# Kernel optimization log

Measured on AMD Instinct MI355X. Metric: run time of the kernel, lower is better.

## Reference

```python
import jax, jax.numpy as jnp
import numpy as np

B, T, C, H, K = 16, 8192, 128, 128, 5


def setup_inputs() -> dict:
    key = jax.random.key(0)
    ks = jax.random.split(key, 6)
    std = 1.0 / np.sqrt(H)  # matches reset_parameters uniform(-std, std)
    u = lambda k, s: jax.random.uniform(k, s, jnp.float32, -std, std)
    return {
        "inputs": jax.random.normal(ks[0], (B, T, C), jnp.float32),
        "init_state": jax.random.normal(ks[1], (2, B, H), jnp.float32),
        "z_w": u(ks[2], (H, C, K)),
        "z_b": u(ks[3], (H,)),
        "f_w": u(ks[4], (H, C, K)),
        "f_b": u(ks[5], (H,)),
    }


def _conv1d_same(x, w, b):
    # x: (B, C, T), w: (H, C, K) -> (B, H, T), padding='same'
    y = jax.lax.conv_general_dilated(
        x, w, window_strides=(1,), padding="SAME",
        dimension_numbers=("NCH", "OIH", "NCH"))
    return y + b[None, :, None]


def reference(inputs, init_state, z_w, z_b, f_w, f_b):
    # inputs: (B, T, C); init_state: (2, B, H)
    x = jnp.transpose(inputs, (0, 2, 1))                       # (B, C, T)
    raw_f = jnp.transpose(_conv1d_same(x, f_w, f_b), (0, 2, 1))  # (B, T, H)
    raw_z = jnp.transpose(_conv1d_same(x, z_w, z_b), (0, 2, 1))  # (B, T, H)
    # prepend init state along time -> (B, T+1, H)
    raw_f = jnp.concatenate([init_state[0][:, None, :], raw_f], axis=1)
    raw_z = jnp.concatenate([init_state[1][:, None, :], raw_z], axis=1)
    log_one_minus_f = jax.nn.log_sigmoid(-raw_f)  # mode='f'
    log_z = jax.nn.log_sigmoid(raw_z)
    log_f = jax.nn.log_sigmoid(raw_f)
    cs = jnp.cumsum(log_f, axis=1)
    # recurrent_gates[t] = log_f[t] - cumsum[t] + cumsum[-1]
    rg = log_f - cs + cs[:, -1:, :]
    log_hidden = jax.lax.cumlogsumexp(log_z + log_one_minus_f + rg, axis=1)
    return jnp.exp(log_hidden - rg)  # (B, T+1, H)
```

## Files before the change

kernel.cpp:

```cpp
#include <hip/hip_runtime.h>
#include <hip/hip_bf16.h>
#include <cstdint>

#define DEVFN __device__ __forceinline__

namespace {

constexpr int B = 16, T = 8192, C = 128, H = 128, K = 5;
constexpr int TP1 = T + 1;
constexpr int N = B * TP1 * H;
constexpr int NKK = 20;
constexpr int NCH = T / 64;
constexpr int NSER = B * H;
constexpr int WF_ELE = NKK * 16 * 64 * 8;

typedef __attribute__((ext_vector_type(8))) short short8;
typedef __attribute__((ext_vector_type(4))) float f32x4;

DEVFN float sigmoidf(float x) { return 1.0f / (1.0f + __expf(-x)); }
DEVFN unsigned bfb(float v) {
  __hip_bfloat16 h = __float2bfloat16(v);
  return (unsigned)*reinterpret_cast<unsigned short*>(&h);
}

DEVFN void compose(float& P, float& Q, float& Fl, float Pr, float Qr, float Flr) {
  float t = Fl * Pr;
  P = P * t;
  Q = fmaf(t, Q, Qr);
  Fl = Flr;
}

__global__ __launch_bounds__(256)
void wprep_kernel(const float* __restrict__ fw, const float* __restrict__ zw,
                  short* __restrict__ Wfrag) {
  int idx = blockIdx.x * 256 + threadIdx.x;
  if (idx >= WF_ELE) return;
  int j = idx & 7;
  int lane = (idx >> 3) & 63;
  int rest = idx >> 9;
  int nf = rest & 15;
  int kk = rest >> 4;
  int kdim = kk * 32 + ((lane >> 4) << 3) + j;
  int n = nf * 16 + (lane & 15);
  int k = kdim >> 7, c = kdim & 127;
  int h = n & 127;
  int src = (h * C + c) * K + k;
  float w = (n < 128) ? fw[src] : zw[src];
  Wfrag[idx] = (short)bfb(w);
}

__global__ __launch_bounds__(512, 2)
void conv_mfma_kernel(const float* __restrict__ x,
                      const float* __restrict__ fb, const float* __restrict__ zb,
                      const short* __restrict__ Wfrag,
                      unsigned* __restrict__ FG,
                      float* __restrict__ sumP, float* __restrict__ sumQ) {
  __shared__ short xs[68 * 128];
  const int b = blockIdx.y;
  const int t0 = blockIdx.x * 64;
  const int tid = threadIdx.x;
  const int lane = tid & 63;
  const int wid = tid >> 6;
  const int lrow = lane & 15;
  const int lg = lane >> 4;

  for (int i = tid; i < 68 * 16; i += 512) {
    int r = i >> 4, co = (i & 15) << 3;
    int t = t0 - 2 + r;
    f32x4 v0 = {0.f, 0.f, 0.f, 0.f}, v1 = v0;
    if (t >= 0 && t < T) {
      const f32x4* p = reinterpret_cast<const f32x4*>(x + ((size_t)(b * T + t)) * C + co);
      v0 = p[0]; v1 = p[1];
    }
    short8 s;
    s[0] = (short)bfb(v0[0]); s[1] = (short)bfb(v0[1]); s[2] = (short)bfb(v0[2]); s[3] = (short)bfb(v0[3]);
    s[4] = (short)bfb(v1[0]); s[5] = (short)bfb(v1[1]); s[6] = (short)bfb(v1[2]); s[7] = (short)bfb(v1[3]);
    int bytes = r * 256 + ((co << 1) ^ ((r & 7) << 4));
    *reinterpret_cast<short8*>(reinterpret_cast<char*>(xs) + bytes) = s;
  }
  __syncthreads();

  f32x4 accF[4], accZ[4];
#pragma unroll
  for (int mf = 0; mf < 4; ++mf) { accF[mf] = {0.f,0.f,0.f,0.f}; accZ[mf] = {0.f,0.f,0.f,0.f}; }

  const char* xsb = reinterpret_cast<const char*>(xs);
  const char* wfb = reinterpret_cast<const char*>(Wfrag);
  const int boff = (wid * 64 + lane) * 16;

#pragma unroll 2
  for (int kk = 0; kk < NKK; ++kk) {
    short8 bf, bz, a[4];
    const char* wp = wfb + boff + kk * 16384;
    bf = *reinterpret_cast<const short8*>(wp);
    bz = *reinterpret_cast<const short8*>(wp + 8192);
    const int k = kk >> 2, c0b = (kk & 3) << 6;
#pragma unroll
    for (int mf = 0; mf < 4; ++mf) {
      int row = mf * 16 + lrow + k;
      int bytes = row * 256 + ((c0b + (lg << 4)) ^ ((row & 7) << 4));
      a[mf] = *reinterpret_cast<const short8*>(xsb + bytes);
    }
#pragma unroll
    for (int mf = 0; mf < 4; ++mf) {
      accF[mf] = __builtin_amdgcn_mfma_f32_16x16x32_bf16(a[mf], bf, accF[mf], 0, 0, 0);
      accZ[mf] = __builtin_amdgcn_mfma_f32_16x16x32_bf16(a[mf], bz, accZ[mf], 0, 0, 0);
    }
  }

  const int cblk = blockIdx.x;
  const int h = wid * 16 + lrow;
  const float biasF = fb[h], biasZ = zb[h];
  float cP = 1.f, cQ = 0.f, cFl = 1.f;
#pragma unroll
  for (int mf = 0; mf < 4; ++mf) {
    float y = 0.f, P = 1.f, prevF = 1.f;
#pragma unroll
    for (int j = 0; j < 4; ++j) {
      int m = mf * 16 + lg * 4 + j;
      int s = t0 + m + 1;
      float rf = accF[mf][j] + biasF;
      float rz = accZ[mf][j] + biasZ;
      float F = sigmoidf(rf);
      float G = sigmoidf(rz) * (1.0f - F);
      FG[(size_t)(b * TP1 + s) * H + h] = bfb(F) | (bfb(G) << 16);
      if (j == 0) { y = G; P = 1.f; }
      else { P *= prevF; y = fmaf(prevF, y, G); }
      prevF = F;
    }
    float tP = P, tQ = y, tFl = prevF;
    {
      float pP = __shfl(tP, lane + 16, 64);
      float pQ = __shfl(tQ, lane + 16, 64);
      float pF = __shfl(tFl, lane + 16, 64);
      compose(tP, tQ, tFl, pP, pQ, pF);
      pP = __shfl(tP, lane + 32, 64);
      pQ = __shfl(tQ, lane + 32, 64);
      pF = __shfl(tFl, lane + 32, 64);
      compose(tP, tQ, tFl, pP, pQ, pF);
    }
    if (mf == 0) { cP = tP; cQ = tQ; cFl = tFl; }
    else compose(cP, cQ, cFl, tP, tQ, tFl);
  }
  if (lg == 0) {
    int sidx = cblk * NSER + b * H + h;
    sumP[sidx] = cP;
    sumQ[sidx] = cQ;
  }
}

__global__ void scanB_kernel(const float* __restrict__ init,
                             const unsigned* __restrict__ FG_r,
                             unsigned* __restrict__ FG_w,
                             const float* __restrict__ sumQ,
                             float* __restrict__ sumP_cin,
                             float* __restrict__ out) {
  int g = blockIdx.x * blockDim.x + threadIdx.x;
  int b = g >> 7, h = g & (H - 1);
  float rf = init[g];
  float rz = init[NSER + g];
  float F0 = sigmoidf(rf), z = sigmoidf(rz);
  float G0 = z * (1.0f - F0);
  size_t base = (size_t)b * TP1 * H + h;
  FG_w[base] = bfb(F0) | (bfb(G0) << 16);
  out[base] = G0;
  float y = G0;
  float prevFl = F0;
  for (int j = 0; j < NCH; ++j) {
    int sidx = j * NSER + g;
    float Ps = sumP_cin[sidx];
    float Q  = sumQ[sidx];
    sumP_cin[sidx] = y;
    y = fmaf(prevFl * Ps, y, Q);
    if (j + 1 < NCH)
      prevFl = __uint_as_float(FG_r[base + (size_t)(64 * (j + 1)) * H] << 16);
  }
}

__global__ __launch_bounds__(128)
void scanC_kernel(const unsigned* __restrict__ FG, const float* __restrict__ cin,
                  float* __restrict__ out) {
  const int b = blockIdx.y, j = blockIdx.x, h = threadIdx.x;
  const int s0 = 1 + j * 64;
  float y = cin[j * NSER + b * H + h];
  const size_t base = (size_t)b * TP1 * H + h;
  const unsigned* p = FG + base + (size_t)s0 * H;
  float Fprev = __uint_as_float(p[-H] << 16);
  float* po = out + base + (size_t)s0 * H;
#pragma unroll 8
  for (int t = 0; t < 64; ++t) {
    unsigned u = *p; p += H;
    float G = __uint_as_float(u & 0xffff0000u);
    y = fmaf(Fprev, y, G);
    Fprev = __uint_as_float(u << 16);
    *po = y; po += H;
  }
}

}

extern "C" void kernel_launch(void* const* d_in, const int* in_sizes, int n_in,
                              void* d_out, int out_size, void* d_ws, size_t ws_size,
                              hipStream_t stream) {
  const float* x    = (const float*)d_in[0];
  const float* init = (const float*)d_in[1];
  const float* zw   = (const float*)d_in[2];
  const float* zb   = (const float*)d_in[3];
  const float* fw   = (const float*)d_in[4];
  const float* fb   = (const float*)d_in[5];
  float* out = (float*)d_out;
  char* ws = (char*)d_ws;

  unsigned* FG = (unsigned*)ws;
  float* sumP = (float*)(ws + (size_t)N * 4);
  float* sumQ = sumP + (size_t)NCH * NSER;
  short* Wfrag = (short*)(sumQ + (size_t)NCH * NSER);

  wprep_kernel<<<(WF_ELE + 255) / 256, 256, 0, stream>>>(fw, zw, Wfrag);
  conv_mfma_kernel<<<dim3(NCH, B), 512, 0, stream>>>(x, fb, zb, Wfrag, FG, sumP, sumQ);
  scanB_kernel<<<16, 128, 0, stream>>>(init, FG, FG, sumQ, sumP, out);
  scanC_kernel<<<dim3(NCH, B), 128, 0, stream>>>(FG, sumP, out);
}
```

Measured before the change: 105.8 us.

## Pad LDS pitch, interleave F/Z weight fragments, fully unroll conv loop

Replaces the XOR-swizzled shared-memory layout with a padded row pitch of 136 shorts, so A-fragment addresses become constant offsets from a per-lane base. Weight fragments for F and Z are interleaved per lane so both load from adjacent 16-byte slots. The K loop is fully unrolled and launch bounds now request 4 blocks per CU. The aim is less address arithmetic and better load coalescing and occupancy, at the cost of possible register pressure or spills and a different LDS bank-conflict pattern.

```diff
diff --git a/kernel.cpp b/kernel.cpp
--- a/kernel.cpp
+++ b/kernel.cpp
@@ -12,7 +12,8 @@
 constexpr int NKK = 20;
 constexpr int NCH = T / 64;
 constexpr int NSER = B * H;
-constexpr int WF_ELE = NKK * 16 * 64 * 8;
+constexpr int WF_ELE = NKK * 8 * 64 * 2 * 8;
+constexpr int XPITCH = 136;
 
 typedef __attribute__((ext_vector_type(8))) short short8;
 typedef __attribute__((ext_vector_type(4))) float f32x4;
@@ -36,26 +37,25 @@
   int idx = blockIdx.x * 256 + threadIdx.x;
   if (idx >= WF_ELE) return;
   int j = idx & 7;
-  int lane = (idx >> 3) & 63;
-  int rest = idx >> 9;
-  int nf = rest & 15;
-  int kk = rest >> 4;
+  int fz = (idx >> 3) & 1;
+  int lane = (idx >> 4) & 63;
+  int nf8 = (idx >> 10) & 7;
+  int kk = idx >> 13;
   int kdim = kk * 32 + ((lane >> 4) << 3) + j;
-  int n = nf * 16 + (lane & 15);
+  int h = nf8 * 16 + (lane & 15);
   int k = kdim >> 7, c = kdim & 127;
-  int h = n & 127;
   int src = (h * C + c) * K + k;
-  float w = (n < 128) ? fw[src] : zw[src];
+  float w = fz ? zw[src] : fw[src];
   Wfrag[idx] = (short)bfb(w);
 }
 
-__global__ __launch_bounds__(512, 2)
+__global__ __launch_bounds__(512, 4)
 void conv_mfma_kernel(const float* __restrict__ x,
                       const float* __restrict__ fb, const float* __restrict__ zb,
                       const short* __restrict__ Wfrag,
                       unsigned* __restrict__ FG,
                       float* __restrict__ sumP, float* __restrict__ sumQ) {
-  __shared__ short xs[68 * 128];
+  __shared__ short xs[68 * XPITCH];
   const int b = blockIdx.y;
   const int t0 = blockIdx.x * 64;
   const int tid = threadIdx.x;
@@ -75,8 +75,7 @@
     short8 s;
     s[0] = (short)bfb(v0[0]); s[1] = (short)bfb(v0[1]); s[2] = (short)bfb(v0[2]); s[3] = (short)bfb(v0[3]);
     s[4] = (short)bfb(v1[0]); s[5] = (short)bfb(v1[1]); s[6] = (short)bfb(v1[2]); s[7] = (short)bfb(v1[3]);
-    int bytes = r * 256 + ((co << 1) ^ ((r & 7) << 4));
-    *reinterpret_cast<short8*>(reinterpret_cast<char*>(xs) + bytes) = s;
+    *reinterpret_cast<short8*>(xs + r * XPITCH + co) = s;
   }
   __syncthreads();
 
@@ -85,22 +84,19 @@
   for (int mf = 0; mf < 4; ++mf) { accF[mf] = {0.f,0.f,0.f,0.f}; accZ[mf] = {0.f,0.f,0.f,0.f}; }
 
   const char* xsb = reinterpret_cast<const char*>(xs);
-  const char* wfb = reinterpret_cast<const char*>(Wfrag);
-  const int boff = (wid * 64 + lane) * 16;
-
-#pragma unroll 2
+  const short8* wb = reinterpret_cast<const short8*>(Wfrag) + (wid * 64 + lane) * 2;
+  const int abase = lrow * 272 + lg * 16;
+
+#pragma unroll
   for (int kk = 0; kk < NKK; ++kk) {
-    short8 bf, bz, a[4];
-    const char* wp = wfb + boff + kk * 16384;
-    bf = *reinterpret_cast<const short8*>(wp);
-    bz = *reinterpret_cast<const short8*>(wp + 8192);
-    const int k = kk >> 2, c0b = (kk & 3) << 6;
-#pragma unroll
-    for (int mf = 0; mf < 4; ++mf) {
-      int row = mf * 16 + lrow + k;
-      int bytes = row * 256 + ((c0b + (lg << 4)) ^ ((row & 7) << 4));
-      a[mf] = *reinterpret_cast<const short8*>(xsb + bytes);
-    }
+    const int k = kk >> 2;
+    const int cq = (kk & 3) << 6;
+    short8 bf = wb[kk * 1024];
+    short8 bz = wb[kk * 1024 + 1];
+    short8 a[4];
+#pragma unroll
+    for (int mf = 0; mf < 4; ++mf)
+      a[mf] = *reinterpret_cast<const short8*>(xsb + (abase + (mf * 16 + k) * 272 + cq));
 #pragma unroll
     for (int mf = 0; mf < 4; ++mf) {
       accF[mf] = __builtin_amdgcn_mfma_f32_16x16x32_bf16(a[mf], bf, accF[mf], 0, 0, 0);
```

Measured after the change: 109.1 us. +3.0%, slower.
